# Performance work log

Measured on AMD Instinct MI355X. Metric: run time of the kernel, lower is better.

The kernel has to match this reference:

```python
import jax, jax.numpy as jnp
import numpy as np

N_USERS = 20000
N_ITEMS = 30000
N = N_USERS + N_ITEMS          # total nodes
D = 64                          # embedding_dim
EXTRA = 1152                    # 768 metadata + 384 review
E = 500000                      # full-graph edges
NC = 100                        # clusters
HEADS = 2                       # per-layer GATConv heads
CG_HEADS = 4                    # GlobalGATOverClusters hard-codes heads=4
L = 2                           # num_layers
ED = 2                          # edge_dim


def _gat(x, ei, ea, lin, a_src, a_dst, lin_e, a_edge, bias, heads, nnodes):
    """PyG GATConv: add self loops (edge_attr fill='mean'), concat=False -> head mean."""
    C = a_src.shape[-1]
    loop = jnp.arange(nnodes)
    src = jnp.concatenate([ei[0], loop])
    dst = jnp.concatenate([ei[1], loop])
    ea_full = jnp.concatenate([ea, jnp.broadcast_to(ea.mean(0), (nnodes, ea.shape[1]))], 0)
    xh = (x @ lin).reshape(nnodes, heads, C)            # [N,H,C]
    asrc = (xh * a_src).sum(-1)                         # [N,H]
    adst = (xh * a_dst).sum(-1)
    eh = (ea_full @ lin_e).reshape(-1, heads, C)        # [Etot,H,C]
    ae = (eh * a_edge).sum(-1)                          # [Etot,H]
    al = jax.nn.leaky_relu(asrc[src] + adst[dst] + ae, 0.2)
    amax = jax.ops.segment_max(al, dst, num_segments=nnodes)
    ex = jnp.exp(al - amax[dst])
    s = jax.ops.segment_sum(ex, dst, num_segments=nnodes)
    w = ex / (s[dst] + 1e-16)
    out = jax.ops.segment_sum(xh[src] * w[..., None], dst, num_segments=nnodes)
    return out.mean(1) + bias


def _graph_norm(x, weight, bias, mean_scale, eps=1e-5):
    mean = x.mean(0)
    out = x - mean_scale * mean
    var = (out * out).mean(0)
    return weight * out * jax.lax.rsqrt(var + eps) + bias


def _forward(product_extra_features, user_emb, item_emb, fus_w1, fus_b1, fus_w2, fus_b2,
             full_edge_attr, gcn_w, gcn_b,
             cg_lin, cg_att_src, cg_att_dst, cg_lin_edge, cg_att_edge, cg_bias, cluster_edge_attr,
             gat_lin, gat_att_src, gat_att_dst, gat_lin_edge, gat_att_edge, gat_bias,
             gn_weight, gn_bias, gn_mean_scale,
             full_edge_index, cluster_assignment, cluster_edge_index):
    # fusion MLP on item side (dropout is identity at inference)
    h = jnp.maximum(jnp.concatenate([item_emb, product_extra_features], -1) @ fus_w1 + fus_b1, 0.0)
    enriched_items = h @ fus_w2 + fus_b2
    X = jnp.concatenate([user_emb, enriched_items], 0)  # [N, D]

    # per-cluster GCN == one GCN over intra-cluster edges + self loops;
    # nodes in clusters with zero intra edges keep original features
    ei0, ei1 = full_edge_index[0], full_edge_index[1]
    intra = cluster_assignment[ei0] == cluster_assignment[ei1]
    loop = jnp.arange(N)
    row = jnp.concatenate([ei0, loop])
    col = jnp.concatenate([ei1, loop])
    ew = jnp.concatenate([intra.astype(X.dtype), jnp.ones((N,), X.dtype)])
    deg = jax.ops.segment_sum(ew, col, num_segments=N)
    dinv = jnp.where(deg > 0, jax.lax.rsqrt(deg), 0.0)
    norm = dinv[row] * ew * dinv[col]
    xw = X @ gcn_w
    gcn_out = jax.ops.segment_sum(xw[row] * norm[:, None], col, num_segments=N) + gcn_b
    cl_has_edge = jax.ops.segment_sum(intra.astype(jnp.int32), cluster_assignment[ei0], num_segments=NC) > 0
    Xc = jnp.where(cl_has_edge[cluster_assignment][:, None], gcn_out, X)

    # mean pool per cluster
    cnt = jax.ops.segment_sum(jnp.ones((N,), X.dtype), cluster_assignment, num_segments=NC)
    pooled = jax.ops.segment_sum(Xc, cluster_assignment, num_segments=NC) / jnp.maximum(cnt, 1.0)[:, None]

    # global GAT over clusters (inter-cluster multigraph, precomputed)
    cl_upd = _gat(pooled, cluster_edge_index, cluster_edge_attr,
                  cg_lin, cg_att_src, cg_att_dst, cg_lin_edge, cg_att_edge, cg_bias, CG_HEADS, NC)
    Xcomb = Xc + cl_upd[cluster_assignment]

    # full-graph GAT stack with GraphNorm + residual ELU (dropout identity)
    for i in range(L):
        Xin = Xcomb
        g = _gat(Xcomb, full_edge_index, full_edge_attr,
                 gat_lin[i], gat_att_src[i], gat_att_dst[i],
                 gat_lin_edge[i], gat_att_edge[i], gat_bias[i], HEADS, N)
        g = _graph_norm(g, gn_weight[i], gn_bias[i], gn_mean_scale[i])
        Xcomb = jax.nn.elu(g + Xin)

    return Xcomb[:N_USERS], Xcomb[N_USERS:]


def setup_inputs() -> dict:
    rng = np.random.default_rng(0)
    fei = rng.integers(0, N, size=(2, E)).astype(np.int32)
    ca = rng.integers(0, NC, size=(N,)).astype(np.int32)
    fea = rng.random((E, ED)).astype(np.float32)
    # build_cluster_graph: one cluster edge per inter-cluster full edge
    cu, cv = ca[fei[0]], ca[fei[1]]
    m = cu != cv
    cei = np.stack([cu[m], cv[m]]).astype(np.int32)
    cea = fea[m]

    key = jax.random.key(0)
    ks = jax.random.split(key, 24)
    nrm = lambda k, shp, s=0.05: jax.random.normal(k, shp, dtype=jnp.float32) * s
    return {
        'product_extra_features': jax.random.normal(ks[0], (N_ITEMS, EXTRA), dtype=jnp.float32),
        'user_emb': nrm(ks[1], (N_USERS, D), 1.0),
        'item_emb': nrm(ks[2], (N_ITEMS, D), 1.0),
        'fus_w1': nrm(ks[3], (D + EXTRA, 2 * D)),
        'fus_b1': jnp.zeros((2 * D,), jnp.float32),
        'fus_w2': nrm(ks[4], (2 * D, D)),
        'fus_b2': jnp.zeros((D,), jnp.float32),
        'full_edge_attr': jnp.asarray(fea),
        'gcn_w': nrm(ks[5], (D, D)),
        'gcn_b': jnp.zeros((D,), jnp.float32),
        'cg_lin': nrm(ks[6], (D, CG_HEADS * D)),
        'cg_att_src': nrm(ks[7], (CG_HEADS, D)),
        'cg_att_dst': nrm(ks[8], (CG_HEADS, D)),
        'cg_lin_edge': nrm(ks[9], (ED, CG_HEADS * D)),
        'cg_att_edge': nrm(ks[10], (CG_HEADS, D)),
        'cg_bias': jnp.zeros((D,), jnp.float32),
        'cluster_edge_attr': jnp.asarray(cea),
        'gat_lin': nrm(ks[11], (L, D, HEADS * D)),
        'gat_att_src': nrm(ks[12], (L, HEADS, D)),
        'gat_att_dst': nrm(ks[13], (L, HEADS, D)),
        'gat_lin_edge': nrm(ks[14], (L, ED, HEADS * D)),
        'gat_att_edge': nrm(ks[15], (L, HEADS, D)),
        'gat_bias': jnp.zeros((L, D), jnp.float32),
        'gn_weight': jnp.ones((L, D), jnp.float32),
        'gn_bias': jnp.zeros((L, D), jnp.float32),
        'gn_mean_scale': jnp.ones((L, D), jnp.float32),
        'full_edge_index': jnp.asarray(fei),
        'cluster_assignment': jnp.asarray(ca),
        'cluster_edge_index': jnp.asarray(cei),
    }


def reference(product_extra_features, user_emb, item_emb, fus_w1, fus_b1, fus_w2, fus_b2,
              full_edge_attr, gcn_w, gcn_b,
              cg_lin, cg_att_src, cg_att_dst, cg_lin_edge, cg_att_edge, cg_bias, cluster_edge_attr,
              gat_lin, gat_att_src, gat_att_dst, gat_lin_edge, gat_att_edge, gat_bias,
              gn_weight, gn_bias, gn_mean_scale,
              full_edge_index, cluster_assignment, cluster_edge_index):
    return _forward(product_extra_features, user_emb, item_emb, fus_w1, fus_b1, fus_w2, fus_b2,
                    full_edge_attr, gcn_w, gcn_b,
                    cg_lin, cg_att_src, cg_att_dst, cg_lin_edge, cg_att_edge, cg_bias, cluster_edge_attr,
                    gat_lin, gat_att_src, gat_att_dst, gat_lin_edge, gat_att_edge, gat_bias,
                    gn_weight, gn_bias, gn_mean_scale,
                    full_edge_index, cluster_assignment, cluster_edge_index)
```

## Files before the change

kernel.cpp:

```cpp
#include <hip/hip_runtime.h>
#include <hip/hip_bf16.h>

#define N_USERS 20000
#define N_ITEMS 30000
#define NTOT    50000
#define DIM     64
#define EXTRA_D 1152
#define E_EDGES 500000
#define NC      100
#define KTOT    1216
#define KSTEPS  38
#define PPART   16
#define SPART   128

#define B_FEI  1954
#define B_W1   608
#define B_W2   32
#define B_CEI  256
#define PREP_GRID (B_FEI+B_W1+B_W2+B_CEI)

#define FUS_BLKS ((N_ITEMS+127)/128)
#define SCAN1_BLKS ((NTOT+1023)/1024)
#define B_COPY 1250
#define B_CC   64
#define FUS_GRID (FUS_BLKS+SCAN1_BLKS+1+B_COPY+B_CC)

#define SC3_BLKS ((NTOT+255)/256)
#define FILL_BLKS ((E_EDGES+255)/256)
#define DEG_BLKS ((NTOT+3)/4)

typedef __attribute__((ext_vector_type(8))) short short8;
typedef __attribute__((ext_vector_type(4))) float v4f;

__device__ __forceinline__ float wred_sum(float v){
#pragma unroll
  for(int o=32;o;o>>=1) v += __shfl_xor(v,o,64);
  return v;
}
__device__ __forceinline__ int wred_sumi(int v){
#pragma unroll
  for(int o=32;o;o>>=1) v += __shfl_xor(v,o,64);
  return v;
}
__device__ __forceinline__ float lrelu(float x){ return x>0.f? x : 0.2f*x; }
__device__ __forceinline__ short f2bf(float f){
  unsigned u=__float_as_uint(f);
  unsigned r=(u + 0x7FFFu + ((u>>16)&1u))>>16;
  return (short)r;
}
__device__ __forceinline__ unsigned pack_bf2(float x, float y){
  return (unsigned)(unsigned short)f2bf(x) | ((unsigned)(unsigned short)f2bf(y)<<16);
}

__global__ __launch_bounds__(256) void prep_edges_kernel(
    const float* __restrict__ w1, short* __restrict__ w1t,
    const float* __restrict__ w2, short* __restrict__ w2t,
    const int* __restrict__ ca,
    const int* __restrict__ fei, const float* __restrict__ fea,
    int* __restrict__ cnt_dst, int* __restrict__ clflag, int* __restrict__ degI,
    float2* __restrict__ partA,
    const int* __restrict__ cei, const float* __restrict__ cea, int Ec,
    int* __restrict__ ccnt_dst, float2* __restrict__ partB)
{
  __shared__ int hist[NC];
  __shared__ float2 w4[4];
  const int b=blockIdx.x, t=threadIdx.x;
  const int lane=t&63, wv=t>>6;
  if(b < B_FEI){
    int e = b*256+t;
    float a0=0.f,a1=0.f;
    if(e<E_EDGES){
      int s=fei[e], d=fei[E_EDGES+e];
      atomicAdd(&cnt_dst[d],1);
      int cs=ca[s];
      if(cs==ca[d]){ clflag[cs]=1; atomicAdd(&degI[d],1); }
      float2 v=*(const float2*)(fea+2*e);
      a0=v.x; a1=v.y;
    }
    a0=wred_sum(a0); a1=wred_sum(a1);
    if(lane==0) w4[wv]=make_float2(a0,a1);
    __syncthreads();
    if(t==0){ float2 r=w4[0]; for(int i=1;i<4;i++){r.x+=w4[i].x; r.y+=w4[i].y;} partA[b]=r; }
  } else if(b < B_FEI+B_W1){
    int i = (b-B_FEI)*256+t;
    int row = i>>7, n = i&127;
    int s = row>>5, kk = row&31;
    w1t[s*4096 + n*32 + kk] = f2bf(w1[i]);
  } else if(b < B_FEI+B_W1+B_W2){
    int i = (b-B_FEI-B_W1)*256+t;
    int n = i>>6, c = i&63;
    w2t[c*128 + n] = f2bf(w2[i]);
  } else {
    int bb = b-(B_FEI+B_W1+B_W2);
    for(int i=t;i<NC;i+=256) hist[i]=0;
    __syncthreads();
    float a0=0.f,a1=0.f;
    for(int e=bb*256+t; e<Ec; e+=B_CEI*256){
      atomicAdd(&hist[cei[Ec+e]],1);
      float2 v=*(const float2*)(cea+2*e);
      a0+=v.x; a1+=v.y;
    }
    a0=wred_sum(a0); a1=wred_sum(a1);
    if(lane==0) w4[wv]=make_float2(a0,a1);
    __syncthreads();
    if(t==0){ float2 r=w4[0]; for(int i=1;i<4;i++){r.x+=w4[i].x; r.y+=w4[i].y;} partB[bb]=r; }
    for(int i=t;i<NC;i+=256) if(hist[i]) atomicAdd(&ccnt_dst[i],hist[i]);
  }
}

__global__ __launch_bounds__(256) void fus_scan_kernel(
    const float* __restrict__ item, const float* __restrict__ extra,
    const short* __restrict__ w1t, const float* __restrict__ b1,
    const short* __restrict__ w2t, const float* __restrict__ b2,
    float* __restrict__ X,
    const float2* __restrict__ partA, const float2* __restrict__ partB, int Ec,
    const float* __restrict__ cg_le, const float* __restrict__ cg_ae,
    const float* __restrict__ gat_le, const float* __restrict__ gat_ae,
    float* __restrict__ coefs,
    const int* __restrict__ cnt_dst, int* __restrict__ incl, int* __restrict__ bsum,
    const float* __restrict__ u, const int* __restrict__ ca, int* __restrict__ ccnt)
{
  __shared__ short As[128*40];
  __shared__ short Bs[128*40];
  __shared__ short Hs[128*136];
  __shared__ int ssc[256];
  const int tid = threadIdx.x;
  const int b = blockIdx.x;
  if(b < FUS_BLKS){
    const int blk = b;
    const int w = tid>>6, lane = tid&63, quad = lane>>4, l16 = lane&15;
    const int mw = w&1, nw = w>>1;

    v4f acc[4][4];
#pragma unroll
    for(int a=0;a<4;a++)
#pragma unroll
      for(int c=0;c<4;c++) acc[a][c] = (v4f){0.f,0.f,0.f,0.f};

    const int arow = tid>>3;
    const int aoff = (tid&7)*4;
    for(int s=0;s<KSTEPS;s++){
      const int k0 = s*32;
#pragma unroll
      for(int it=0;it<4;it++){
        int r = arow + it*32;
        int col = k0 + aoff;
        int gr = blk*128 + r; if(gr >= N_ITEMS) gr = N_ITEMS-1;
        float4 v = (col < DIM) ? *(const float4*)(item + (size_t)gr*DIM + col)
                               : *(const float4*)(extra + (size_t)gr*EXTRA_D + (col-DIM));
        short4 bv; bv.x=f2bf(v.x); bv.y=f2bf(v.y); bv.z=f2bf(v.z); bv.w=f2bf(v.w);
        *(short4*)&As[r*40 + aoff] = bv;
      }
#pragma unroll
      for(int it=0;it<2;it++){
        int idx = tid + it*256;
        int4 v = *(const int4*)(w1t + (size_t)s*4096 + idx*8);
        int n = idx>>2, kk = (idx&3)*8;
        *(int4*)&Bs[n*40 + kk] = v;
      }
      __syncthreads();
      short8 af[4], bf_[4];
#pragma unroll
      for(int i=0;i<4;i++){
        int m = mw*64 + i*16 + l16;
        af[i]  = *(const short8*)&As[m*40 + quad*8];
        int n = nw*64 + i*16 + l16;
        bf_[i] = *(const short8*)&Bs[n*40 + quad*8];
      }
#pragma unroll
      for(int mi=0;mi<4;mi++)
#pragma unroll
        for(int ni=0;ni<4;ni++)
          acc[mi][ni] = __builtin_amdgcn_mfma_f32_16x16x32_bf16(af[mi], bf_[ni], acc[mi][ni], 0,0,0);
      __syncthreads();
    }

#pragma unroll
    for(int ni=0;ni<4;ni++){
      int n = nw*64 + ni*16 + l16;
      float bias = b1[n];
#pragma unroll
      for(int mi=0;mi<4;mi++){
        int mbase = mw*64 + mi*16 + quad*4;
#pragma unroll
        for(int r=0;r<4;r++){
          float hv = fmaxf(acc[mi][ni][r] + bias, 0.f);
          Hs[(mbase+r)*136 + n] = f2bf(hv);
        }
      }
    }
    __syncthreads();

    v4f acc2[2][4];
#pragma unroll
    for(int a=0;a<2;a++)
#pragma unroll
      for(int c=0;c<4;c++) acc2[a][c] = (v4f){0.f,0.f,0.f,0.f};
#pragma unroll
    for(int ks=0;ks<4;ks++){
      short8 ha[2];
#pragma unroll
      for(int mi=0;mi<2;mi++){
        int m = w*32 + mi*16 + l16;
        ha[mi] = *(const short8*)&Hs[m*136 + ks*32 + quad*8];
      }
#pragma unroll
      for(int ni=0;ni<4;ni++){
        int c = ni*16 + l16;
        short8 wb = *(const short8*)(w2t + c*128 + ks*32 + quad*8);
#pragma unroll
        for(int mi=0;mi<2;mi++)
          acc2[mi][ni] = __builtin_amdgcn_mfma_f32_16x16x32_bf16(ha[mi], wb, acc2[mi][ni], 0,0,0);
      }
    }
#pragma unroll
    for(int ni=0;ni<4;ni++){
      int c = ni*16 + l16;
      float b2v = b2[c];
#pragma unroll
      for(int mi=0;mi<2;mi++){
        int mbase = w*32 + mi*16 + quad*4;
#pragma unroll
        for(int r=0;r<4;r++){
          int row = blk*128 + mbase + r;
          if(row < N_ITEMS) X[(size_t)(N_USERS+row)*64 + c] = acc2[mi][ni][r] + b2v;
        }
      }
    }
  } else if(b < FUS_BLKS+SCAN1_BLKS){
    int sb = b-FUS_BLKS;
    int base = sb*1024 + tid*4;
    int a0=(base  <NTOT)?cnt_dst[base  ]+1:0;
    int a1=(base+1<NTOT)?cnt_dst[base+1]+1:0;
    int a2=(base+2<NTOT)?cnt_dst[base+2]+1:0;
    int a3=(base+3<NTOT)?cnt_dst[base+3]+1:0;
    int l1=a0+a1, l2=l1+a2, l3=l2+a3;
    ssc[tid]=l3; __syncthreads();
    for(int off=1;off<256;off<<=1){
      int v=(tid>=off)?ssc[tid-off]:0; __syncthreads();
      ssc[tid]+=v; __syncthreads();
    }
    int prev = tid? ssc[tid-1]:0;
    if(base  <NTOT) incl[base  ]=prev+a0;
    if(base+1<NTOT) incl[base+1]=prev+l1;
    if(base+2<NTOT) incl[base+2]=prev+l2;
    if(base+3<NTOT) incl[base+3]=prev+l3;
    if(tid==255) bsum[sb]=ssc[255];
  } else if(b == FUS_BLKS+SCAN1_BLKS){
    int lane=tid&63; int wv=tid>>6;
    {
      int hh=wv;
      float v0 = cg_le[hh*64+lane]*cg_ae[hh*64+lane];
      float v1 = cg_le[256 + hh*64+lane]*cg_ae[hh*64+lane];
      v0=wred_sum(v0); v1=wred_sum(v1);
      if(lane==0){ coefs[8+hh]=v0; coefs[12+hh]=v1; }
    }
    {
      int l=wv>>1, hh=wv&1;
      float v0 = gat_le[l*256 + hh*64+lane]     * gat_ae[l*128+hh*64+lane];
      float v1 = gat_le[l*256 + 128 + hh*64+lane]* gat_ae[l*128+hh*64+lane];
      v0=wred_sum(v0); v1=wred_sum(v1);
      if(lane==0){ coefs[16+l*2+hh]=v0; coefs[20+l*2+hh]=v1; }
    }
    __syncthreads();
    if(wv==0){
      float sx=0.f, sy=0.f;
      for(int i=lane;i<B_FEI;i+=64){ float2 v=partA[i]; sx+=v.x; sy+=v.y; }
      sx=wred_sum(sx); sy=wred_sum(sy);
      if(lane==0){ coefs[4]=sx/(float)E_EDGES; coefs[5]=sy/(float)E_EDGES; }
    }
    if(wv==1){
      float sx=0.f, sy=0.f;
      for(int i=lane;i<B_CEI;i+=64){ float2 v=partB[i]; sx+=v.x; sy+=v.y; }
      sx=wred_sum(sx); sy=wred_sum(sy);
      if(lane==0){ coefs[6]=sx/(float)Ec; coefs[7]=sy/(float)Ec; }
    }
  } else if(b < FUS_BLKS+SCAN1_BLKS+1+B_COPY){
    int i = (b-FUS_BLKS-SCAN1_BLKS-1)*256+tid;
    ((float4*)X)[i] = ((const float4*)u)[i];
  } else {
    __shared__ int hist2[NC];
    int bb = b-(FUS_BLKS+SCAN1_BLKS+1+B_COPY);
    for(int i=tid;i<NC;i+=256) hist2[i]=0;
    __syncthreads();
    for(int n=bb*256+tid; n<NTOT; n+=B_CC*256) atomicAdd(&hist2[ca[n]],1);
    __syncthreads();
    for(int i=tid;i<NC;i+=256) if(hist2[i]) atomicAdd(&ccnt[i],hist2[i]);
  }
}

__global__ __launch_bounds__(256) void mid_kernel(
    const int* __restrict__ incl, const int* __restrict__ cnt,
    const int* __restrict__ bsum, int* __restrict__ offs, int* __restrict__ fillptr,
    const float* __restrict__ coefs, int2* __restrict__ slot2,
    const int* __restrict__ degI, float* __restrict__ dinv,
    const int* __restrict__ ccnt_dst, int* __restrict__ coffs, int* __restrict__ cfillp,
    const float* __restrict__ X, const float* __restrict__ gw, float* __restrict__ xw)
{
  __shared__ float Wl[64*64];
  __shared__ float rowb[4][64];
  __shared__ int sprev;
  const int b=blockIdx.x, t=threadIdx.x;
  if(b < SC3_BLKS){
    int blk10 = b>>2;
    if(t<64){
      int v = (t<blk10)? bsum[t] : 0;
      v = wred_sumi(v);
      if(t==0) sprev=v;
    }
    __syncthreads();
    unsigned pk = pack_bf2(coefs[4], coefs[5]);
    int i = b*256+t;
    if(i<NTOT){
      int c=cnt[i];
      int start = sprev + incl[i] - (c+1);
      offs[i]=start; fillptr[i]=start;
      slot2[start+c]=make_int2(i,(int)pk);
      dinv[i]=rsqrtf((float)(degI[i]+1));
    }
    if(i==0) offs[NTOT]=E_EDGES+NTOT;
  } else if(b == SC3_BLKS){
    if(t<64){
      int lane=t;
      int v0 = (2*lane<NC)? ccnt_dst[2*lane]:0;
      int v1 = (2*lane+1<NC)? ccnt_dst[2*lane+1]:0;
      int pair=v0+v1;
      int sc=pair;
#pragma unroll
      for(int o=1;o<64;o<<=1){ int t2=__shfl_up(sc,o,64); if(lane>=o) sc+=t2; }
      int excl = sc - pair;
      if(2*lane<NC){ coffs[2*lane]=excl; cfillp[2*lane]=excl; }
      if(2*lane+1<NC){ coffs[2*lane+1]=excl+v0; cfillp[2*lane+1]=excl+v0; }
      if(lane==63) coffs[NC]=sc;
    }
  } else {
    int bb=b-SC3_BLKS-1;
    const int lane=t&63, wv=t>>6;
    for(int i=t;i<4096;i+=256) Wl[i]=gw[i];
    __syncthreads();
    for(int r=bb*4+wv; r<NTOT; r+=1024*4){
      rowb[wv][lane]=X[(size_t)r*64+lane];
      float acc=0.f;
#pragma unroll 8
      for(int k=0;k<64;k++) acc+=rowb[wv][k]*Wl[k*64+lane];
      xw[(size_t)r*64+lane]=acc;
    }
  }
}

__global__ __launch_bounds__(256) void fill_kernel(
    const int* __restrict__ fei, const float* __restrict__ fea,
    int* __restrict__ fillptr, int2* __restrict__ slot2,
    const int* __restrict__ cei, const float* __restrict__ cea, int Ec,
    int* __restrict__ cfillp, int* __restrict__ cslot_src, float2* __restrict__ cslot_ea)
{
  __shared__ int hist[NC];
  __shared__ int base[NC];
  const int b=blockIdx.x, t=threadIdx.x;
  if(b<FILL_BLKS){
    int e=b*256+t;
    if(e<E_EDGES){
      int dst=fei[E_EDGES+e], src=fei[e];
      int pos=atomicAdd(&fillptr[dst],1);
      float2 v=*(const float2*)(fea+2*e);
      slot2[pos]=make_int2(src,(int)pack_bf2(v.x,v.y));
    }
  } else {
    int bb=b-FILL_BLKS;
    const int chunk=(Ec+127)/128;
    const int beg=bb*chunk;
    const int end=min(beg+chunk,Ec);
    for(int i=t;i<NC;i+=256) hist[i]=0;
    __syncthreads();
    for(int e=beg+t;e<end;e+=256) atomicAdd(&hist[cei[Ec+e]],1);
    __syncthreads();
    for(int i=t;i<NC;i+=256){
      int h=hist[i];
      base[i] = h ? atomicAdd(&cfillp[i],h) : 0;
      hist[i]=0;
    }
    __syncthreads();
    for(int e=beg+t;e<end;e+=256){
      int d=cei[Ec+e];
      int pos = base[d] + atomicAdd(&hist[d],1);
      cslot_src[pos]=cei[e];
      cslot_ea[pos]=make_float2(cea[2*e],cea[2*e+1]);
    }
  }
}

__global__ __launch_bounds__(256) void gcn_agg_kernel(const float* __restrict__ X,
    const float* __restrict__ xw, const float* __restrict__ gcn_b,
    const int* __restrict__ offs, const int2* __restrict__ slot2, const int* __restrict__ ca,
    const float* __restrict__ dinv, const int* __restrict__ flag,
    float* __restrict__ Xc, float* __restrict__ psum){
  __shared__ float2 stg[4][64];
  int lane=threadIdx.x&63, wv=threadIdx.x>>6;
  int n=blockIdx.x*4+wv;
  int beg=offs[n], end=offs[n+1], myca=ca[n];
  float acc=0.f;
  for(int c0=beg;c0<end;c0+=64){
    int j=c0+lane;
    float coef=0.f; int s=0;
    if(j<end){
      s=slot2[j].x;
      if(ca[s]==myca) coef=dinv[s];
    }
    stg[wv][lane]=make_float2(__int_as_float(s),coef);
    unsigned long long bal=__ballot(coef!=0.f);
    while(bal){
      int k=__builtin_ctzll(bal); bal&=bal-1;
      float2 sc=stg[wv][k];
      acc += sc.y * xw[(size_t)__float_as_int(sc.x)*64+lane];
    }
  }
  float gout = dinv[n]*acc + gcn_b[lane];
  float xc = flag[myca] ? gout : X[(size_t)n*64+lane];
  Xc[(size_t)n*64+lane]=xc;
  atomicAdd(&psum[(size_t)(blockIdx.x&(PPART-1))*NC*64 + myca*64+lane], xc);
}

__global__ __launch_bounds__(256) void cluster_all_kernel(
    const float* __restrict__ psum, const int* __restrict__ ccnt,
    const float* __restrict__ cg_lin, const float* __restrict__ as_, const float* __restrict__ ad_,
    const int* __restrict__ coffs, const int* __restrict__ cslot_src, const float2* __restrict__ cslot_ea,
    const float* __restrict__ coefs, const float* __restrict__ cg_bias, float* __restrict__ cl_upd)
{
  __shared__ float pool[NC*64];
  __shared__ float sas[NC*4];
  __shared__ float sad[4];
  __shared__ float sW[NC*4];
  __shared__ float Ps[4][64], Pd[4][64];
  __shared__ float qq[4][64];
  __shared__ float ssum[4];
  __shared__ float red[4][64];
  const int c=blockIdx.x, t=threadIdx.x;
  const int lane=t&63, hh=t>>6;
  for(int i=t;i<NC*64;i+=256){
    float a=0.f;
#pragma unroll
    for(int p=0;p<PPART;p++) a += psum[(size_t)p*NC*64 + i];
    pool[i]=a/fmaxf((float)ccnt[i>>6],1.f);
  }
  {
    float av=as_[hh*64+lane], dv=ad_[hh*64+lane];
    for(int k=0;k<64;k++){
      float cl=cg_lin[k*256+hh*64+lane];
      float s=wred_sum(cl*av);
      float d=wred_sum(cl*dv);
      if(lane==0){ Ps[hh][k]=s; Pd[hh][k]=d; }
    }
  }
  for(int i=t;i<NC*4;i+=256) sW[i]=0.f;
  __syncthreads();
  for(int i=t;i<NC*4;i+=256){
    int s=i>>2, h=i&3;
    float a=0.f;
#pragma unroll 8
    for(int k=0;k<64;k++) a += pool[s*64+k]*Ps[h][k];
    sas[i]=a;
  }
  if(t<4){
    float a=0.f;
#pragma unroll 8
    for(int k=0;k<64;k++) a += pool[c*64+k]*Pd[t][k];
    sad[t]=a;
  }
  __syncthreads();
  float ad4[4], A0[4], A1[4];
#pragma unroll
  for(int h=0;h<4;h++){ ad4[h]=sad[h]; A0[h]=coefs[8+h]; A1[h]=coefs[12+h]; }
  const int beg=coffs[c], end=coffs[c+1];
  for(int j=beg+t;j<end;j+=256){
    int s=cslot_src[j]; float2 e=cslot_ea[j];
#pragma unroll
    for(int h=0;h<4;h++){
      float al=lrelu(sas[s*4+h]+ad4[h]+e.x*A0[h]+e.y*A1[h]);
      atomicAdd(&sW[s*4+h], __expf(al));
    }
  }
  if(t<4){
    float al=lrelu(sas[c*4+t]+ad4[t]+coefs[6]*A0[t]+coefs[7]*A1[t]);
    atomicAdd(&sW[c*4+t], __expf(al));
  }
  __syncthreads();
  {
    float p=0.f;
    if(lane<NC)    p += sW[lane*4+hh];
    if(lane+64<NC) p += sW[(lane+64)*4+hh];
    p=wred_sum(p);
    if(lane==0) ssum[hh]=p+1e-16f;
  }
  {
    float a=0.f;
    for(int s=0;s<NC;s++) a += sW[s*4+hh]*pool[s*64+lane];
    qq[hh][lane]=a;
  }
  __syncthreads();
  {
    float inv=1.f/ssum[hh];
    float a=0.f;
#pragma unroll 4
    for(int k=0;k<64;k++) a += qq[hh][k]*cg_lin[k*256+hh*64+lane];
    red[hh][lane]=a*inv;
  }
  __syncthreads();
  if(t<64) cl_upd[c*64+t]=0.25f*(red[0][t]+red[1][t]+red[2][t]+red[3][t])+cg_bias[t];
}

__global__ __launch_bounds__(256) void gat_xh0_kernel(const float* __restrict__ Xc,
    const float* __restrict__ cl_upd, const int* __restrict__ ca,
    const float* __restrict__ lin, const float* __restrict__ att_s, const float* __restrict__ att_d,
    float2* __restrict__ xh2, float* __restrict__ asrc, float* __restrict__ adst,
    float* __restrict__ Xa){
  __shared__ __align__(16) float Wl[64*128];
  __shared__ float rowb[4][64];
  int t=threadIdx.x;
  for(int i=t;i<8192;i+=256) Wl[i]=lin[i];
  __syncthreads();
  int lane=t&63, wv=t>>6;
  float as0=att_s[lane], as1=att_s[64+lane], ad0=att_d[lane], ad1=att_d[64+lane];
  for(int r=blockIdx.x*4+wv; r<NTOT; r+=gridDim.x*4){
    float xv = Xc[(size_t)r*64+lane] + cl_upd[ca[r]*64+lane];
    Xa[(size_t)r*64+lane]=xv;
    rowb[wv][lane]=xv;
    float x0=0.f,x1=0.f;
#pragma unroll 8
    for(int k=0;k<64;k++){ float q=rowb[wv][k]; x0+=q*Wl[k*128+lane]; x1+=q*Wl[k*128+64+lane]; }
    xh2[(size_t)r*64+lane]=make_float2(x0,x1);
    float p0=wred_sum(x0*as0);
    float p1=wred_sum(x1*as1);
    float q0=wred_sum(x0*ad0);
    float q1=wred_sum(x1*ad1);
    if(lane==0){ asrc[2*r]=p0; asrc[2*r+1]=p1; adst[2*r]=q0; adst[2*r+1]=q1; }
  }
}
__global__ __launch_bounds__(256) void gat_xh1_kernel(const float* __restrict__ g,
    const float* __restrict__ Xres, const float* __restrict__ spart,
    const float* __restrict__ gnw, const float* __restrict__ gnb, const float* __restrict__ gnms,
    const float* __restrict__ lin, const float* __restrict__ att_s, const float* __restrict__ att_d,
    float2* __restrict__ xh2, float* __restrict__ asrc, float* __restrict__ adst,
    float* __restrict__ Xb){
  __shared__ __align__(16) float Wl[64*128];
  __shared__ float rowb[4][64];
  __shared__ float sm[4][64], sv[4][64];
  int t=threadIdx.x;
  int lane=t&63, wv=t>>6;
  for(int i=t;i<8192;i+=256) Wl[i]=lin[i];
  {
    float a0=0.f,a1=0.f;
    for(int p=wv;p<SPART;p+=4){ a0+=spart[p*128+lane]; a1+=spart[p*128+64+lane]; }
    sm[wv][lane]=a0; sv[wv][lane]=a1;
  }
  __syncthreads();
  const float invN = 1.f/(float)NTOT;
  float m=(sm[0][lane]+sm[1][lane]+sm[2][lane]+sm[3][lane])*invN;
  float vsum=(sv[0][lane]+sv[1][lane]+sv[2][lane]+sv[3][lane])*invN;
  float mm=gnms[lane]*m;
  float gwv=rsqrtf(vsum - 2.f*mm*m + mm*mm + 1e-5f)*gnw[lane];
  float gbv=gnb[lane];
  float as0=att_s[lane], as1=att_s[64+lane], ad0=att_d[lane], ad1=att_d[64+lane];
  for(int r=blockIdx.x*4+wv; r<NTOT; r+=gridDim.x*4){
    float z=(g[(size_t)r*64+lane]-mm)*gwv+gbv + Xres[(size_t)r*64+lane];
    float xv = z>0.f? z : __expf(z)-1.f;
    Xb[(size_t)r*64+lane]=xv;
    rowb[wv][lane]=xv;
    float x0=0.f,x1=0.f;
#pragma unroll 8
    for(int k=0;k<64;k++){ float q=rowb[wv][k]; x0+=q*Wl[k*128+lane]; x1+=q*Wl[k*128+64+lane]; }
    xh2[(size_t)r*64+lane]=make_float2(x0,x1);
    float p0=wred_sum(x0*as0);
    float p1=wred_sum(x1*as1);
    float q0=wred_sum(x0*ad0);
    float q1=wred_sum(x1*ad1);
    if(lane==0){ asrc[2*r]=p0; asrc[2*r+1]=p1; adst[2*r]=q0; adst[2*r+1]=q1; }
  }
}

__global__ __launch_bounds__(256) void gat_agg_kernel(const float2* __restrict__ xh2,
    const float2* __restrict__ asrc, const float2* __restrict__ adst,
    const int* __restrict__ offs, const int2* __restrict__ slot2,
    const float* __restrict__ coefs, int layer, const float* __restrict__ bias,
    float* __restrict__ g, float* __restrict__ spart){
  __shared__ float4 stg[4][64];
  __shared__ float s1[64], s2[64];
  int t=threadIdx.x;
  int lane=t&63, wv=t>>6;
  if(t<64){ s1[t]=0.f; s2[t]=0.f; }
  __syncthreads();
  int n=blockIdx.x*4+wv;
  float A00=coefs[16+layer*2+0], A01=coefs[16+layer*2+1];
  float A10=coefs[20+layer*2+0], A11=coefs[20+layer*2+1];
  int beg=offs[n], end=offs[n+1];
  float2 adn=adst[n];
  float s0=0.f,sB=0.f,acc0=0.f,acc1=0.f;
  for(int c0=beg;c0<end;c0+=64){
    int j=c0+lane;
    float ex0=0.f,ex1=0.f; int s=0;
    if(j<end){
      int2 sl=slot2[j];
      s=sl.x;
      unsigned p=(unsigned)sl.y;
      float e0=__uint_as_float(p<<16);
      float e1=__uint_as_float(p&0xffff0000u);
      float2 a=asrc[s];
      ex0=__expf(lrelu(a.x+adn.x+e0*A00+e1*A10));
      ex1=__expf(lrelu(a.y+adn.y+e0*A01+e1*A11));
    }
    s0+=ex0; sB+=ex1;
    stg[wv][lane]=make_float4(__int_as_float(s),ex0,ex1,0.f);
    int cnt=min(64,end-c0);
    int k=0;
    for(; k+4<=cnt; k+=4){
      float4 w0=stg[wv][k], w1=stg[wv][k+1], w2=stg[wv][k+2], w3=stg[wv][k+3];
      float2 x0=xh2[(size_t)__float_as_int(w0.x)*64+lane];
      float2 x1=xh2[(size_t)__float_as_int(w1.x)*64+lane];
      float2 x2=xh2[(size_t)__float_as_int(w2.x)*64+lane];
      float2 x3=xh2[(size_t)__float_as_int(w3.x)*64+lane];
      acc0 += w0.y*x0.x + w1.y*x1.x + w2.y*x2.x + w3.y*x3.x;
      acc1 += w0.z*x0.y + w1.z*x1.y + w2.z*x2.y + w3.z*x3.y;
    }
    for(; k<cnt; k++){
      float4 ws=stg[wv][k];
      float2 xv=xh2[(size_t)__float_as_int(ws.x)*64+lane];
      acc0 += ws.y*xv.x;
      acc1 += ws.z*xv.y;
    }
  }
  s0=wred_sum(s0); sB=wred_sum(sB);
  float gv = 0.5f*(acc0/(s0+1e-16f)+acc1/(sB+1e-16f))+bias[lane];
  g[(size_t)n*64+lane]=gv;
  atomicAdd(&s1[lane],gv);
  atomicAdd(&s2[lane],gv*gv);
  __syncthreads();
  float* dstp = spart + (size_t)(blockIdx.x&(SPART-1))*128;
  if(t<64) atomicAdd(&dstp[t],s1[t]);
  else if(t<128) atomicAdd(&dstp[t],s2[t-64]);
}

__global__ __launch_bounds__(256) void gnorm_elu_kernel(const float* __restrict__ g,
    const float* __restrict__ Xin, const float* __restrict__ spart,
    const float* __restrict__ gw, const float* __restrict__ gb, const float* __restrict__ gms,
    float* __restrict__ outp){
  __shared__ float sst[2][128];
  const float invN = 1.f/(float)NTOT;
  int t=threadIdx.x;
  {
    int d=t&127, hf=t>>7;
    float a=0.f;
    for(int p=hf*64;p<hf*64+64;p++) a+=spart[p*128+d];
    sst[hf][d]=a;
  }
  __syncthreads();
  int i0=blockIdx.x*256+t;
  int d0=(i0&15)*4;
  float mmv[4],gwv[4],gbv[4];
#pragma unroll
  for(int j=0;j<4;j++){
    int d=d0+j;
    float m=(sst[0][d]+sst[1][d])*invN;
    float mm=gms[d]*m;
    mmv[j]=mm;
    gwv[j]=rsqrtf((sst[0][64+d]+sst[1][64+d])*invN-2.f*mm*m+mm*mm+1e-5f)*gw[d];
    gbv[j]=gb[d];
  }
  for(int i=i0;i<NTOT*16;i+=gridDim.x*256){
    float4 gv=((const float4*)g)[i];
    float4 xv=((const float4*)Xin)[i];
    float4 o; float z;
    z=(gv.x-mmv[0])*gwv[0]+gbv[0]+xv.x; o.x = z>0.f? z : __expf(z)-1.f;
    z=(gv.y-mmv[1])*gwv[1]+gbv[1]+xv.y; o.y = z>0.f? z : __expf(z)-1.f;
    z=(gv.z-mmv[2])*gwv[2]+gbv[2]+xv.z; o.z = z>0.f? z : __expf(z)-1.f;
    z=(gv.w-mmv[3])*gwv[3]+gbv[3]+xv.w; o.w = z>0.f? z : __expf(z)-1.f;
    ((float4*)outp)[i]=o;
  }
}

extern "C" void kernel_launch(void* const* d_in, const int* in_sizes, int n_in,
                              void* d_out, int out_size, void* d_ws, size_t ws_size,
                              hipStream_t stream)
{
  const float* extra = (const float*)d_in[0];
  const float* user  = (const float*)d_in[1];
  const float* item  = (const float*)d_in[2];
  const float* fw1 = (const float*)d_in[3];
  const float* fb1 = (const float*)d_in[4];
  const float* fw2 = (const float*)d_in[5];
  const float* fb2 = (const float*)d_in[6];
  const float* fea = (const float*)d_in[7];
  const float* gcn_w = (const float*)d_in[8];
  const float* gcn_b = (const float*)d_in[9];
  const float* cg_lin = (const float*)d_in[10];
  const float* cg_as = (const float*)d_in[11];
  const float* cg_ad = (const float*)d_in[12];
  const float* cg_le = (const float*)d_in[13];
  const float* cg_ae = (const float*)d_in[14];
  const float* cg_bias = (const float*)d_in[15];
  const float* cea = (const float*)d_in[16];
  const float* gat_lin = (const float*)d_in[17];
  const float* gat_as = (const float*)d_in[18];
  const float* gat_ad = (const float*)d_in[19];
  const float* gat_le = (const float*)d_in[20];
  const float* gat_ae = (const float*)d_in[21];
  const float* gat_bias = (const float*)d_in[22];
  const float* gn_w = (const float*)d_in[23];
  const float* gn_b = (const float*)d_in[24];
  const float* gn_ms = (const float*)d_in[25];
  const int* fei = (const int*)d_in[26];
  const int* ca  = (const int*)d_in[27];
  const int* cei = (const int*)d_in[28];
  const int Ec = in_sizes[16]/2;
  float* outp = (float*)d_out;

  char* w = (char*)d_ws;
  auto alloc=[&](size_t b)->char*{ char* p=w; w += (b+255)&~(size_t)255; return p; };

  char* z0 = w;
  int* cnt_dst = (int*)alloc((size_t)NTOT*4);
  int* degI = (int*)alloc((size_t)NTOT*4);
  int* clflag = (int*)alloc(NC*4);
  int* ccnt = (int*)alloc(NC*4);
  int* ccnt_dst = (int*)alloc(NC*4);
  float* psum = (float*)alloc((size_t)PPART*NC*64*4);
  float* spart0 = (float*)alloc((size_t)SPART*128*4);
  float* spart1 = (float*)alloc((size_t)SPART*128*4);
  size_t zbytes = (size_t)(w - z0);

  float2* partA = (float2*)alloc(2048*8);
  float2* partB = (float2*)alloc(256*8);
  float* coefs = (float*)alloc(32*4);
  int* offs = (int*)alloc((size_t)(NTOT+1)*4);
  int* incl = (int*)alloc((size_t)NTOT*4);
  int* bsum = (int*)alloc(64*4);
  int* fillptr = (int*)alloc((size_t)NTOT*4);
  int2* slot2 = (int2*)alloc((size_t)(E_EDGES+NTOT)*8);
  int* coffs = (int*)alloc((size_t)(NC+1)*4);
  int* cfillp = (int*)alloc((size_t)NC*4);
  int* cslot_src = (int*)alloc((size_t)E_EDGES*4);
  float2* cslot_ea = (float2*)alloc((size_t)E_EDGES*8);
  float* dinv = (float*)alloc((size_t)NTOT*4);
  float* cl_upd = (float*)alloc(NC*64*4);
  float* asrc = (float*)alloc((size_t)NTOT*2*4);
  float* adst = (float*)alloc((size_t)NTOT*2*4);
  short* w1t = (short*)alloc((size_t)KSTEPS*4096*2);
  short* w2t = (short*)alloc((size_t)64*128*2);
  float* bufA = (float*)alloc((size_t)NTOT*64*4);
  float* bufB = (float*)alloc((size_t)NTOT*64*4);
  float* bufC = (float*)alloc((size_t)NTOT*64*4);
  float* bufD = (float*)alloc((size_t)NTOT*64*4);
  float* bufE = (float*)alloc((size_t)NTOT*128*4);

  float* X  = bufA; float* g  = bufA;
  float* Xc = bufB;
  float* xw = bufC; float* Xb = bufC;
  float* Xa = bufD;
  float2* xh2 = (float2*)bufE;

  hipMemsetAsync(z0, 0, zbytes, stream);

  prep_edges_kernel<<<PREP_GRID,256,0,stream>>>(fw1, w1t, fw2, w2t, ca,
                                              fei, fea, cnt_dst, clflag, degI, partA,
                                              cei, cea, Ec, ccnt_dst, partB);
  fus_scan_kernel<<<FUS_GRID,256,0,stream>>>(item, extra, w1t, fb1, w2t, fb2, X,
                                              partA, partB, Ec, cg_le, cg_ae, gat_le, gat_ae, coefs,
                                              cnt_dst, incl, bsum, user, ca, ccnt);
  mid_kernel<<<SC3_BLKS+1+1024,256,0,stream>>>(incl, cnt_dst, bsum, offs, fillptr, coefs, slot2,
                                              degI, dinv, ccnt_dst, coffs, cfillp,
                                              X, gcn_w, xw);
  fill_kernel<<<FILL_BLKS+128,256,0,stream>>>(fei, fea, fillptr, slot2,
                                              cei, cea, Ec, cfillp, cslot_src, cslot_ea);

  gcn_agg_kernel<<<DEG_BLKS,256,0,stream>>>(X, xw, gcn_b, offs, slot2, ca, dinv, clflag, Xc, psum);
  cluster_all_kernel<<<NC,256,0,stream>>>(psum, ccnt, cg_lin, cg_as, cg_ad,
                                          coffs, cslot_src, cslot_ea, coefs, cg_bias, cl_upd);

  gat_xh0_kernel<<<1024,256,0,stream>>>(Xc, cl_upd, ca, gat_lin, gat_as, gat_ad,
                                        xh2, asrc, adst, Xa);
  gat_agg_kernel<<<DEG_BLKS,256,0,stream>>>(xh2, (const float2*)asrc, (const float2*)adst,
                                            offs, slot2, coefs, 0, gat_bias, g, spart0);
  gat_xh1_kernel<<<1024,256,0,stream>>>(g, Xa, spart0, gn_w, gn_b, gn_ms,
                                        gat_lin+64*128, gat_as+128, gat_ad+128,
                                        xh2, asrc, adst, Xb);
  gat_agg_kernel<<<DEG_BLKS,256,0,stream>>>(xh2, (const float2*)asrc, (const float2*)adst,
                                            offs, slot2, coefs, 1, gat_bias+64, g, spart1);
  gnorm_elu_kernel<<<512,256,0,stream>>>(g, Xb, spart1, gn_w+64, gn_b+64, gn_ms+64, outp);
}
```

Baseline: 731.3 us.

## Split cluster GAT into per-cluster projection and aggregation kernels

Replaces the single cluster kernel, in which every block recomputed pooling of all 100 clusters and the attention projections, with a prep kernel where each block pools and projects only its own cluster (xh, asrc, adst), followed by an aggregation kernel that reads those precomputed values. This removes redundant per-block work (each block summed the full partial buffer and ran 64 serial reductions). It costs an extra kernel launch and a global round-trip for the small intermediate buffers.

```diff
diff --git a/kernel.cpp b/kernel.cpp
--- a/kernel.cpp
+++ b/kernel.cpp
@@ -420,90 +420,68 @@
   atomicAdd(&psum[(size_t)(blockIdx.x&(PPART-1))*NC*64 + myca*64+lane], xc);
 }
 
-__global__ __launch_bounds__(256) void cluster_all_kernel(
-    const float* __restrict__ psum, const int* __restrict__ ccnt,
-    const float* __restrict__ cg_lin, const float* __restrict__ as_, const float* __restrict__ ad_,
+__global__ __launch_bounds__(256) void cluster_prep_kernel(const float* __restrict__ psum,
+    const int* __restrict__ ccnt, const float* __restrict__ cg_lin,
+    const float* __restrict__ as_, const float* __restrict__ ad_,
+    float* __restrict__ xh_c, float* __restrict__ asrc_c, float* __restrict__ adst_c){
+  __shared__ float prow[64];
+  const int c=blockIdx.x, t=threadIdx.x;
+  if(t<64){
+    float a=0.f;
+#pragma unroll
+    for(int p=0;p<PPART;p++) a += psum[(size_t)p*NC*64 + c*64 + t];
+    prow[t]=a/fmaxf((float)ccnt[c],1.f);
+  }
+  __syncthreads();
+  float acc=0.f;
+#pragma unroll 8
+  for(int k=0;k<64;k++) acc += prow[k]*cg_lin[k*256+t];
+  xh_c[c*256+t]=acc;
+  int lane=t&63, hh=t>>6;
+  float s=wred_sum(acc*as_[hh*64+lane]);
+  float d=wred_sum(acc*ad_[hh*64+lane]);
+  if(lane==0){ asrc_c[c*4+hh]=s; adst_c[c*4+hh]=d; }
+}
+__global__ __launch_bounds__(256) void cluster_agg_kernel(
     const int* __restrict__ coffs, const int* __restrict__ cslot_src, const float2* __restrict__ cslot_ea,
-    const float* __restrict__ coefs, const float* __restrict__ cg_bias, float* __restrict__ cl_upd)
+    const float* __restrict__ asrc_c, const float* __restrict__ adst_c, const float* __restrict__ coefs,
+    const float* __restrict__ xh_c, const float* __restrict__ cg_bias, float* __restrict__ cl_upd)
 {
-  __shared__ float pool[NC*64];
   __shared__ float sas[NC*4];
-  __shared__ float sad[4];
   __shared__ float sW[NC*4];
-  __shared__ float Ps[4][64], Pd[4][64];
-  __shared__ float qq[4][64];
   __shared__ float ssum[4];
   __shared__ float red[4][64];
   const int c=blockIdx.x, t=threadIdx.x;
-  const int lane=t&63, hh=t>>6;
-  for(int i=t;i<NC*64;i+=256){
-    float a=0.f;
-#pragma unroll
-    for(int p=0;p<PPART;p++) a += psum[(size_t)p*NC*64 + i];
-    pool[i]=a/fmaxf((float)ccnt[i>>6],1.f);
-  }
-  {
-    float av=as_[hh*64+lane], dv=ad_[hh*64+lane];
-    for(int k=0;k<64;k++){
-      float cl=cg_lin[k*256+hh*64+lane];
-      float s=wred_sum(cl*av);
-      float d=wred_sum(cl*dv);
-      if(lane==0){ Ps[hh][k]=s; Pd[hh][k]=d; }
-    }
-  }
-  for(int i=t;i<NC*4;i+=256) sW[i]=0.f;
-  __syncthreads();
-  for(int i=t;i<NC*4;i+=256){
-    int s=i>>2, h=i&3;
-    float a=0.f;
-#pragma unroll 8
-    for(int k=0;k<64;k++) a += pool[s*64+k]*Ps[h][k];
-    sas[i]=a;
-  }
-  if(t<4){
-    float a=0.f;
-#pragma unroll 8
-    for(int k=0;k<64;k++) a += pool[c*64+k]*Pd[t][k];
-    sad[t]=a;
-  }
-  __syncthreads();
-  float ad4[4], A0[4], A1[4];
-#pragma unroll
-  for(int h=0;h<4;h++){ ad4[h]=sad[h]; A0[h]=coefs[8+h]; A1[h]=coefs[12+h]; }
+  for(int i=t;i<NC*4;i+=256){ sas[i]=asrc_c[i]; sW[i]=0.f; }
+  __syncthreads();
+  float ad[4], A0[4], A1[4];
+#pragma unroll
+  for(int h=0;h<4;h++){ ad[h]=adst_c[c*4+h]; A0[h]=coefs[8+h]; A1[h]=coefs[12+h]; }
   const int beg=coffs[c], end=coffs[c+1];
   for(int j=beg+t;j<end;j+=256){
     int s=cslot_src[j]; float2 e=cslot_ea[j];
 #pragma unroll
     for(int h=0;h<4;h++){
-      float al=lrelu(sas[s*4+h]+ad4[h]+e.x*A0[h]+e.y*A1[h]);
+      float al=lrelu(sas[s*4+h]+ad[h]+e.x*A0[h]+e.y*A1[h]);
       atomicAdd(&sW[s*4+h], __expf(al));
     }
   }
   if(t<4){
-    float al=lrelu(sas[c*4+t]+ad4[t]+coefs[6]*A0[t]+coefs[7]*A1[t]);
+    float al=lrelu(sas[c*4+t]+ad[t]+coefs[6]*A0[t]+coefs[7]*A1[t]);
     atomicAdd(&sW[c*4+t], __expf(al));
   }
   __syncthreads();
-  {
-    float p=0.f;
-    if(lane<NC)    p += sW[lane*4+hh];
-    if(lane+64<NC) p += sW[(lane+64)*4+hh];
-    p=wred_sum(p);
-    if(lane==0) ssum[hh]=p+1e-16f;
-  }
-  {
-    float a=0.f;
-    for(int s=0;s<NC;s++) a += sW[s*4+hh]*pool[s*64+lane];
-    qq[hh][lane]=a;
-  }
-  __syncthreads();
-  {
-    float inv=1.f/ssum[hh];
-    float a=0.f;
-#pragma unroll 4
-    for(int k=0;k<64;k++) a += qq[hh][k]*cg_lin[k*256+hh*64+lane];
-    red[hh][lane]=a*inv;
-  }
+  const int h=t>>6, lane=t&63;
+  float p=0.f;
+  if(lane<NC)    p += sW[lane*4+h];
+  if(lane+64<NC) p += sW[(lane+64)*4+h];
+  p=wred_sum(p);
+  if(lane==0) ssum[h]=p+1e-16f;
+  __syncthreads();
+  float inv=1.f/ssum[h];
+  float acc=0.f;
+  for(int s=0;s<NC;s++) acc += sW[s*4+h]*xh_c[s*256+h*64+lane];
+  red[h][lane]=acc*inv;
   __syncthreads();
   if(t<64) cl_upd[c*64+t]=0.25f*(red[0][t]+red[1][t]+red[2][t]+red[3][t])+cg_bias[t];
 }
@@ -739,6 +717,9 @@
   int* cslot_src = (int*)alloc((size_t)E_EDGES*4);
   float2* cslot_ea = (float2*)alloc((size_t)E_EDGES*8);
   float* dinv = (float*)alloc((size_t)NTOT*4);
+  float* xh_c = (float*)alloc(NC*256*4);
+  float* asrc_c = (float*)alloc(NC*4*4);
+  float* adst_c = (float*)alloc(NC*4*4);
   float* cl_upd = (float*)alloc(NC*64*4);
   float* asrc = (float*)alloc((size_t)NTOT*2*4);
   float* adst = (float*)alloc((size_t)NTOT*2*4);
@@ -771,8 +752,9 @@
                                               cei, cea, Ec, cfillp, cslot_src, cslot_ea);
 
   gcn_agg_kernel<<<DEG_BLKS,256,0,stream>>>(X, xw, gcn_b, offs, slot2, ca, dinv, clflag, Xc, psum);
-  cluster_all_kernel<<<NC,256,0,stream>>>(psum, ccnt, cg_lin, cg_as, cg_ad,
-                                          coffs, cslot_src, cslot_ea, coefs, cg_bias, cl_upd);
+  cluster_prep_kernel<<<NC,256,0,stream>>>(psum, ccnt, cg_lin, cg_as, cg_ad, xh_c, asrc_c, adst_c);
+  cluster_agg_kernel<<<NC,256,0,stream>>>(coffs, cslot_src, cslot_ea, asrc_c, adst_c, coefs,
+                                          xh_c, cg_bias, cl_upd);
 
   gat_xh0_kernel<<<1024,256,0,stream>>>(Xc, cl_upd, ca, gat_lin, gat_as, gat_ad,
                                         xh2, asrc, adst, Xa);
```

After: 690.2 us. -5.6%, faster.
